# Optimization experiments

Hardware: AMD Instinct MI355X
Metric: run time of the kernel (lower is better)

## Reference

```python
import jax, jax.numpy as jnp
import numpy as np
from jax import lax

N_WIRES = 4
N_OPS = 30
BN_EPS = 1e-5


def _rl_ops():
    # Deterministic stand-in for tq.RandomLayer(n_ops=30): cycle rx/ry/rz/cnot.
    kinds = ['rx', 'ry', 'rz', 'cnot']
    ops, p = [], 0
    for i in range(N_OPS):
        k = kinds[i % 4]
        if k == 'cnot':
            ops.append((k, i % N_WIRES, (i + 1) % N_WIRES))
        else:
            ops.append((k, i % N_WIRES, p))
            p += 1
    return ops, p

RL_OPS, N_RL_PARAMS = _rl_ops()  # 23 rotation params, 7 cnots


def _rx(t):
    c = jnp.cos(t / 2).astype(jnp.complex64)
    s = (-1j * jnp.sin(t / 2).astype(jnp.complex64))
    return jnp.stack([jnp.stack([c, s], -1), jnp.stack([s, c], -1)], -2)


def _ry(t):
    c = jnp.cos(t / 2).astype(jnp.complex64)
    s = jnp.sin(t / 2).astype(jnp.complex64)
    return jnp.stack([jnp.stack([c, -s], -1), jnp.stack([s, c], -1)], -2)


def _rz(t):
    e = jnp.exp((-1j * t / 2).astype(jnp.complex64))
    z = jnp.zeros_like(e)
    return jnp.stack([jnp.stack([e, z], -1), jnp.stack([z, jnp.conj(e)], -1)], -2)


def _apply_1q(state, U, w):
    # state: [B,2,2,2,2]; U: [2,2] (shared) or [B,2,2] (per-sample)
    s = jnp.moveaxis(state, w + 1, -1)
    if U.ndim == 2:
        s = jnp.einsum('ij,b...j->b...i', U, s)
    else:
        s = jnp.einsum('bij,b...j->b...i', U, s)
    return jnp.moveaxis(s, -1, w + 1)


def _apply_cnot(state, c, t):
    s = jnp.moveaxis(state, (c + 1, t + 1), (-2, -1))
    s = s.at[..., 1, :].set(s[..., 1, ::-1])  # flip target where control==1
    return jnp.moveaxis(s, (-2, -1), (c + 1, t + 1))


# PauliZ expectation table: z[k, w] = +/-1 for basis state k on wire w
_ZTAB = np.array([[1.0 - 2.0 * ((k >> (N_WIRES - 1 - w)) & 1) for w in range(N_WIRES)]
                  for k in range(2 ** N_WIRES)], dtype=np.float32)  # [16,4]


def _conv(x, w, b):
    y = lax.conv_general_dilated(x, w, (1, 1), 'SAME',
                                 dimension_numbers=('NCHW', 'OIHW', 'NCHW'))
    return y + b[None, :, None, None]


def _maxpool2(x):
    return lax.reduce_window(x, -jnp.inf, lax.max, (1, 1, 2, 2), (1, 1, 2, 2), 'VALID')


def setup_inputs() -> dict:
    key = jax.random.key(0)
    ks = jax.random.split(key, 8)
    B = 8192
    return {
        'x': jax.random.normal(ks[0], (B, 1, 28, 28), jnp.float32),
        'conv1_w': jax.random.normal(ks[1], (8, 1, 3, 3), jnp.float32) * 0.1,
        'conv1_b': jnp.zeros((8,), jnp.float32),
        'conv2_w': jax.random.normal(ks[2], (16, 8, 3, 3), jnp.float32) * 0.1,
        'conv2_b': jnp.zeros((16,), jnp.float32),
        'fc1_w': jax.random.normal(ks[3], (64, 784), jnp.float32) * 0.05,
        'fc1_b': jnp.zeros((64,), jnp.float32),
        'fc2_w': jax.random.normal(ks[4], (4, 64), jnp.float32) * 0.1,
        'fc2_b': jnp.zeros((4,), jnp.float32),
        'bn_g': jnp.ones((4,), jnp.float32),
        'bn_b': jnp.zeros((4,), jnp.float32),
        'rl_params': jax.random.uniform(ks[5], (N_RL_PARAMS,), jnp.float32,
                                        -np.pi, np.pi),
    }


def reference(x, conv1_w, conv1_b, conv2_w, conv2_b, fc1_w, fc1_b,
              fc2_w, fc2_b, bn_g, bn_b, rl_params):
    B = x.shape[0]
    # CNN backbone: conv -> relu -> pool -> conv -> relu -> pool
    h = _maxpool2(jax.nn.relu(_conv(x, conv1_w, conv1_b)))          # [B,8,14,14]
    h = _maxpool2(jax.nn.relu(_conv(h, conv2_w, conv2_b)))          # [B,16,7,7]
    flat = h.reshape(B, -1)                                         # [B,784]
    h = jax.nn.relu(flat @ fc1_w.T + fc1_b)                         # [B,64]
    feat = h @ fc2_w.T + fc2_b                                      # [B,4]
    # BatchNorm1d (training mode: batch stats, biased variance)
    mean = feat.mean(0)
    var = feat.var(0)
    feat = (feat - mean) / jnp.sqrt(var + BN_EPS) * bn_g + bn_b
    # Quantum state-vector simulation on 4 wires, |0000> start
    state = jnp.zeros((B, 16), jnp.complex64).at[:, 0].set(1.0)
    state = state.reshape(B, 2, 2, 2, 2)
    # Encoder: RX(feat[:, w]) on wire w
    for w in range(N_WIRES):
        state = _apply_1q(state, _rx(feat[:, w]), w)
    # Random layer: 30 sequential gates with fixed trainable params
    gate_fns = {'rx': _rx, 'ry': _ry, 'rz': _rz}
    for kind, w, q in RL_OPS:
        if kind == 'cnot':
            state = _apply_cnot(state, w, q)
        else:
            state = _apply_1q(state, gate_fns[kind](rl_params[q]), w)
    # MeasureAll(PauliZ)
    probs = jnp.abs(state.reshape(B, 16)) ** 2                      # [B,16]
    return probs @ jnp.asarray(_ZTAB)                               # [B,4]
```

## Files before the change

### kernel.cpp

```cpp
#include <hip/hip_runtime.h>
#include <hip/hip_bf16.h>


#define B_EPS 1e-5f

__global__ void prep_kernel(const float* __restrict__ rl,
                            const float* __restrict__ f1w,
                            float* __restrict__ Uout,
                            float* __restrict__ wT2,
                            float* __restrict__ stats)
{
    if (blockIdx.x == 0) {
        __shared__ float2 U[16][16];
        int t = threadIdx.x;
        int r = t >> 4, cc = t & 15;
        U[r][cc] = (r == cc) ? make_float2(1.f, 0.f) : make_float2(0.f, 0.f);
        stats[t] = 0.f;
        stats[t + 256] = 0.f;
        __syncthreads();
        for (int op = 0; op < 30; op++) {
            int kind = op & 3;
            float2 cur = U[r][cc];
            float2 nv;
            if (kind == 3) {
                float2 part = U[r ^ 8][cc];
                nv = (r & 1) ? part : cur;
            } else {
                int m = 8 >> kind;
                float theta = rl[op - (op >> 2)];
                float ch = cosf(0.5f * theta), sh = sinf(0.5f * theta);
                float2 part = U[r ^ m][cc];
                int br = (r & m) ? 1 : 0;
                float2 gc, gp;
                if (kind == 0)      { gc = make_float2(ch, 0.f);           gp = make_float2(0.f, -sh); }
                else if (kind == 1) { gc = make_float2(ch, 0.f);           gp = make_float2(br ? sh : -sh, 0.f); }
                else                { gc = make_float2(ch, br ? sh : -sh); gp = make_float2(0.f, 0.f); }
                nv.x = gc.x*cur.x - gc.y*cur.y + gp.x*part.x - gp.y*part.y;
                nv.y = gc.x*cur.y + gc.y*cur.x + gp.x*part.y + gp.y*part.x;
            }
            __syncthreads();
            U[r][cc] = nv;
            __syncthreads();
        }
        ((float2*)Uout)[t] = U[r][cc];
    } else {
        int id = (blockIdx.x - 1) * 256 + threadIdx.x;
        if (id < 784 * 64) {
            int k = id >> 6, o = id & 63;
            wT2[(((k >> 2) * 64 + o) << 2) + (k & 3)] = f1w[o * 784 + k];
        }
    }
}

__global__ __launch_bounds__(256) void conv_kernel(
    const float* __restrict__ x,  const float* __restrict__ c1w,
    const float* __restrict__ c1b, const float* __restrict__ c2w,
    const float* __restrict__ c2b, const float* __restrict__ wT2,
    const float* __restrict__ f1b, const float* __restrict__ f2w,
    const float* __restrict__ f2bias, float* __restrict__ feat,
    float* __restrict__ stats)
{
    __shared__ union alignas(16) {
        float xin[2][30 * 32];
        float flat[2][800];
    } u;
    __shared__ union alignas(16) {
        float p1[2][8 * 292];
        struct { float part[4][64]; float hs[2][64]; } fc;
    } pu;
    __shared__ float w1s[8][9], b1s[8], w2s[16][73], b2s[16];

    int t = threadIdx.x;
    int w = t >> 6, lane = t & 63;

    {
        float4 z = make_float4(0.f, 0.f, 0.f, 0.f);
        float4* xz = (float4*)u.xin;
        for (int i = t; i < 2 * 30 * 32 / 4; i += 256) xz[i] = z;
        float4* pz = (float4*)pu.p1;
        for (int i = t; i < 2 * 8 * 292 / 4; i += 256) pz[i] = z;
    }
    if (t < 72) ((float*)w1s)[t] = c1w[t];
    if (t < 8)  b1s[t] = c1b[t];
    for (int i = t; i < 16 * 72; i += 256) w2s[i / 72][i % 72] = c2w[i];
    if (t < 16) b2s[t] = c2b[t];
    __syncthreads();

    {
        const float4* xg = (const float4*)(x + (size_t)blockIdx.x * 2 * 784);
        for (int i = t; i < 392; i += 256) {
            float4 v = xg[i];
            int s = i / 196, q = (i - s * 196) * 4;
            float vv[4] = {v.x, v.y, v.z, v.w};
            #pragma unroll
            for (int j = 0; j < 4; j++) {
                int p = q + j, rr = p / 28, cc = p - rr * 28;
                u.xin[s][(rr + 1) * 32 + cc + 1] = vv[j];
            }
        }
    }
    __syncthreads();

    {
        int s = w >> 1, h = w & 1;
        int c = lane >> 3, g = lane & 7;
        if (g < 7) {
            float wk[9];
            #pragma unroll
            for (int q = 0; q < 9; q++) wk[q] = w1s[c][q];
            float bias = b1s[c];
            const float* xb = &u.xin[s][4 * g];
            float* pout = &pu.p1[s][c * 292];
            for (int ii = 0; ii < 7; ii++) {
                int i = h * 7 + ii;
                const float* r = xb + 2 * i * 32;
                float rv[4][6];
                #pragma unroll
                for (int dr = 0; dr < 4; dr++) {
                    float2 a = *(const float2*)(r + dr * 32);
                    float2 b = *(const float2*)(r + dr * 32 + 2);
                    float2 c2v = *(const float2*)(r + dr * 32 + 4);
                    rv[dr][0] = a.x;  rv[dr][1] = a.y;
                    rv[dr][2] = b.x;  rv[dr][3] = b.y;
                    rv[dr][4] = c2v.x; rv[dr][5] = c2v.y;
                }
                float o[2][4];
                #pragma unroll
                for (int dr = 0; dr < 2; dr++)
                    #pragma unroll
                    for (int j = 0; j < 4; j++) {
                        float acc = bias;
                        #pragma unroll
                        for (int ky = 0; ky < 3; ky++)
                            #pragma unroll
                            for (int kx = 0; kx < 3; kx++)
                                acc = fmaf(wk[ky * 3 + kx], rv[dr + ky][j + kx], acc);
                        o[dr][j] = acc;
                    }
                #pragma unroll
                for (int jj = 0; jj < 2; jj++) {
                    float m = fmaxf(fmaxf(o[0][2 * jj], o[0][2 * jj + 1]),
                                    fmaxf(o[1][2 * jj], o[1][2 * jj + 1]));
                    pout[(i + 1) * 18 + 1 + 2 * g + jj] = fmaxf(m, 0.f);
                }
            }
        }
    }
    __syncthreads();

    {
        int s = w >> 1, h = w & 1;
        int c2 = lane >> 2, g2 = lane & 3;
        int i0 = h * 4;
        float bias = b2s[c2];
        float acc[4][2][4];
        #pragma unroll
        for (int ii = 0; ii < 4; ii++)
            #pragma unroll
            for (int dr = 0; dr < 2; dr++)
                #pragma unroll
                for (int j = 0; j < 4; j++) acc[ii][dr][j] = bias;

        const float* pbase = &pu.p1[s][4 * g2] + i0 * 2 * 18;
        for (int ci = 0; ci < 8; ci++) {
            float wk[9];
            #pragma unroll
            for (int q = 0; q < 9; q++) wk[q] = w2s[c2][ci * 9 + q];
            const float* pc_ = pbase + ci * 292;
            #pragma unroll
            for (int ii = 0; ii < 4; ii++) {
                if (ii < 3 || h == 0) {
                    float rv[4][6];
                    #pragma unroll
                    for (int dr = 0; dr < 4; dr++) {
                        const float* rp = pc_ + (ii * 2 + dr) * 18;
                        float2 a = *(const float2*)rp;
                        float2 b = *(const float2*)(rp + 2);
                        float2 cc = *(const float2*)(rp + 4);
                        rv[dr][0] = a.x;  rv[dr][1] = a.y;
                        rv[dr][2] = b.x;  rv[dr][3] = b.y;
                        rv[dr][4] = cc.x; rv[dr][5] = cc.y;
                    }
                    #pragma unroll
                    for (int dr = 0; dr < 2; dr++)
                        #pragma unroll
                        for (int j = 0; j < 4; j++) {
                            float a2 = acc[ii][dr][j];
                            #pragma unroll
                            for (int ky = 0; ky < 3; ky++)
                                #pragma unroll
                                for (int kx = 0; kx < 3; kx++)
                                    a2 = fmaf(wk[ky * 3 + kx], rv[dr + ky][j + kx], a2);
                            acc[ii][dr][j] = a2;
                        }
                }
            }
        }
        #pragma unroll
        for (int ii = 0; ii < 4; ii++) {
            if (ii < 3 || h == 0) {
                int i = i0 + ii;
                #pragma unroll
                for (int jj = 0; jj < 2; jj++) {
                    int pc = 2 * g2 + jj;
                    if (pc < 7) {
                        float m = fmaxf(fmaxf(acc[ii][0][2 * jj], acc[ii][0][2 * jj + 1]),
                                        fmaxf(acc[ii][1][2 * jj], acc[ii][1][2 * jj + 1]));
                        u.flat[s][c2 * 49 + i * 7 + pc] = fmaxf(m, 0.f);
                    }
                }
            }
        }
    }
    __syncthreads();

    {
        int s = w >> 1, h2 = w & 1;
        const float* fl = u.flat[s];
        const float4* wp4 = (const float4*)wT2 + lane;
        int g0 = h2 * 98;
        float a0 = 0.f, a1 = 0.f;
        #pragma unroll 2
        for (int g = g0; g < g0 + 98; g += 2) {
            float4 wv0 = wp4[(size_t)g * 64];
            float4 f0 = *(const float4*)&fl[4 * g];
            float4 wv1 = wp4[(size_t)(g + 1) * 64];
            float4 f1 = *(const float4*)&fl[4 * (g + 1)];
            a0 = fmaf(f0.x, wv0.x, fmaf(f0.y, wv0.y, fmaf(f0.z, wv0.z, fmaf(f0.w, wv0.w, a0))));
            a1 = fmaf(f1.x, wv1.x, fmaf(f1.y, wv1.y, fmaf(f1.z, wv1.z, fmaf(f1.w, wv1.w, a1))));
        }
        pu.fc.part[w][lane] = a0 + a1;
    }
    __syncthreads();

    if (t < 128) {
        int s = t >> 6, o = t & 63;
        float h = pu.fc.part[2 * s][o] + pu.fc.part[2 * s + 1][o] + f1b[o];
        pu.fc.hs[s][o] = fmaxf(h, 0.f);
    }
    __syncthreads();

    if (t < 8) {
        int s = t >> 2, j = t & 3;
        float a = f2bias[j];
        #pragma unroll
        for (int o = 0; o < 64; o++) a = fmaf(pu.fc.hs[s][o], f2w[j * 64 + o], a);
        feat[((size_t)blockIdx.x * 2 + s) * 4 + j] = a;
        int g = blockIdx.x & 63;
        atomicAdd(&stats[g * 8 + j], a);
        atomicAdd(&stats[g * 8 + 4 + j], a * a);
    }
}

__global__ __launch_bounds__(128) void quantum_kernel(
    const float* __restrict__ feat, const float* __restrict__ Ug,
    const float* __restrict__ stats, const float* __restrict__ bn_g,
    const float* __restrict__ bn_b, float* __restrict__ out, int B)
{
    __shared__ float2 Us[256];
    __shared__ float sm[8];
    int t = threadIdx.x;
    for (int i = t; i < 256; i += 128) Us[i] = ((const float2*)Ug)[i];
    if (t < 8) sm[t] = 0.f;
    __syncthreads();
    {
        float v = stats[t] + stats[t + 128] + stats[t + 256] + stats[t + 384];
        atomicAdd(&sm[t & 7], v);
    }
    __syncthreads();
    int s = blockIdx.x * 128 + t;
    float4 fv = ((const float4*)feat)[s];
    float f[4] = {fv.x, fv.y, fv.z, fv.w};
    float cn[4], sn[4];
    float invB = 1.0f / (float)B;
    #pragma unroll
    for (int w = 0; w < 4; w++) {
        float mean = sm[w] * invB;
        float var  = sm[4 + w] * invB - mean * mean;
        float fh = (f[w] - mean) / sqrtf(var + B_EPS) * bn_g[w] + bn_b[w];
        cn[w] = cosf(0.5f * fh);
        sn[w] = sinf(0.5f * fh);
    }
    float re0[16], im0[16];
    #pragma unroll
    for (int k = 0; k < 16; k++) {
        float mag = ((k & 8) ? sn[0] : cn[0]) * ((k & 4) ? sn[1] : cn[1]) *
                    ((k & 2) ? sn[2] : cn[2]) * ((k & 1) ? sn[3] : cn[3]);
        int m = __popc(k) & 3;
        re0[k] = (m == 0) ? mag : (m == 2) ? -mag : 0.f;
        im0[k] = (m == 1) ? -mag : (m == 3) ? mag : 0.f;
    }
    float o0 = 0.f, o1 = 0.f, o2 = 0.f, o3 = 0.f;
    #pragma unroll
    for (int r = 0; r < 16; r++) {
        float ar = 0.f, ai = 0.f;
        #pragma unroll
        for (int k = 0; k < 16; k++) {
            float2 uu = Us[r * 16 + k];
            ar += uu.x * re0[k] - uu.y * im0[k];
            ai += uu.x * im0[k] + uu.y * re0[k];
        }
        float p = ar * ar + ai * ai;
        o0 += (r & 8) ? -p : p;
        o1 += (r & 4) ? -p : p;
        o2 += (r & 2) ? -p : p;
        o3 += (r & 1) ? -p : p;
    }
    float4 ov = {o0, o1, o2, o3};
    ((float4*)out)[s] = ov;
}

extern "C" void kernel_launch(void* const* d_in, const int* in_sizes, int n_in,
                              void* d_out, int out_size, void* d_ws, size_t ws_size,
                              hipStream_t stream)
{
    const float* x   = (const float*)d_in[0];
    const float* c1w = (const float*)d_in[1];
    const float* c1b = (const float*)d_in[2];
    const float* c2w = (const float*)d_in[3];
    const float* c2b = (const float*)d_in[4];
    const float* f1w = (const float*)d_in[5];
    const float* f1b = (const float*)d_in[6];
    const float* f2w = (const float*)d_in[7];
    const float* f2b = (const float*)d_in[8];
    const float* bng = (const float*)d_in[9];
    const float* bnb = (const float*)d_in[10];
    const float* rl  = (const float*)d_in[11];
    float* out = (float*)d_out;

    int B = in_sizes[0] / 784;

    float* wsf   = (float*)d_ws;
    float* feat  = wsf;
    float* wT2   = feat + (size_t)B * 4;
    float* U     = wT2 + 784 * 64;
    float* stats = U + 512;

    prep_kernel<<<197, 256, 0, stream>>>(rl, f1w, U, wT2, stats);
    conv_kernel<<<B / 2, 256, 0, stream>>>(x, c1w, c1b, c2w, c2b, wT2,
                                           f1b, f2w, f2b, feat, stats);
    quantum_kernel<<<B / 128, 128, 0, stream>>>(feat, U, stats, bng, bnb, out, B);
}
```

Before: 226.6 us.

## Run conv2 as an implicit GEMM on MFMA f16 with packed channel layout

New measurement: 235.2 us. +3.8%, slower.

```diff
diff --git a/kernel.cpp b/kernel.cpp
--- a/kernel.cpp
+++ b/kernel.cpp
@@ -3,6 +3,15 @@
 
 
 #define B_EPS 1e-5f
+
+typedef __attribute__((ext_vector_type(8))) _Float16 half8;
+typedef __attribute__((ext_vector_type(4))) float f32x4;
+
+__device__ inline unsigned pack2h(float lo, float hi) {
+    _Float16 l = (_Float16)lo, h = (_Float16)hi;
+    return (unsigned)__builtin_bit_cast(unsigned short, l) |
+           ((unsigned)__builtin_bit_cast(unsigned short, h) << 16);
+}
 
 __global__ void prep_kernel(const float* __restrict__ rl,
                             const float* __restrict__ f1w,
@@ -62,13 +71,18 @@
 {
     __shared__ union alignas(16) {
         float xin[2][30 * 32];
-        float flat[2][800];
+        struct {
+            _Float16 p1c[2][288 * 8];
+            float flat[2][784];
+        } b;
     } u;
     __shared__ union alignas(16) {
         float p1[2][8 * 292];
+        float c2out[196 * 16];
         struct { float part[4][64]; float hs[2][64]; } fc;
-    } pu;
-    __shared__ float w1s[8][9], b1s[8], w2s[16][73], b2s[16];
+    } v;
+    __shared__ unsigned w2c[12 * 16 * 4];
+    __shared__ float w1s[8][9], b1s[8], b2s[16];
 
     int t = threadIdx.x;
     int w = t >> 6, lane = t & 63;
@@ -77,21 +91,25 @@
         float4 z = make_float4(0.f, 0.f, 0.f, 0.f);
         float4* xz = (float4*)u.xin;
         for (int i = t; i < 2 * 30 * 32 / 4; i += 256) xz[i] = z;
-        float4* pz = (float4*)pu.p1;
+        float4* pz = (float4*)v.p1;
         for (int i = t; i < 2 * 8 * 292 / 4; i += 256) pz[i] = z;
     }
     if (t < 72) ((float*)w1s)[t] = c1w[t];
     if (t < 8)  b1s[t] = c1b[t];
-    for (int i = t; i < 16 * 72; i += 256) w2s[i / 72][i % 72] = c2w[i];
-    if (t < 16) b2s[t] = c2b[t];
-    __syncthreads();
-
+    if (t >= 8 && t < 24) b2s[t - 8] = c2b[t - 8];
+    for (int j = t; j < 576; j += 256) {
+        int tap = j >> 6, r = j & 63, ch = r >> 2, ci2 = r & 3;
+        float lo = c2w[ch * 72 + (2 * ci2) * 9 + tap];
+        float hi = c2w[ch * 72 + (2 * ci2 + 1) * 9 + tap];
+        w2c[(tap * 16 + ch) * 4 + ci2] = pack2h(lo, hi);
+    }
+    if (t < 192) w2c[576 + t] = 0u;
     {
         const float4* xg = (const float4*)(x + (size_t)blockIdx.x * 2 * 784);
         for (int i = t; i < 392; i += 256) {
-            float4 v = xg[i];
+            float4 vv4 = xg[i];
             int s = i / 196, q = (i - s * 196) * 4;
-            float vv[4] = {v.x, v.y, v.z, v.w};
+            float vv[4] = {vv4.x, vv4.y, vv4.z, vv4.w};
             #pragma unroll
             for (int j = 0; j < 4; j++) {
                 int p = q + j, rr = p / 28, cc = p - rr * 28;
@@ -110,7 +128,7 @@
             for (int q = 0; q < 9; q++) wk[q] = w1s[c][q];
             float bias = b1s[c];
             const float* xb = &u.xin[s][4 * g];
-            float* pout = &pu.p1[s][c * 292];
+            float* pout = &v.p1[s][c * 292];
             for (int ii = 0; ii < 7; ii++) {
                 int i = h * 7 + ii;
                 const float* r = xb + 2 * i * 32;
@@ -149,74 +167,109 @@
     __syncthreads();
 
     {
-        int s = w >> 1, h = w & 1;
-        int c2 = lane >> 2, g2 = lane & 3;
-        int i0 = h * 4;
-        float bias = b2s[c2];
-        float acc[4][2][4];
+        unsigned* pc = (unsigned*)u.b.p1c;
+        for (int i = t; i < 2304; i += 256) {
+            int s = i / 1152, r = i - 1152 * s;
+            int pix = r >> 2, c2 = r & 3;
+            float lo = v.p1[s][(2 * c2) * 292 + pix];
+            float hi = v.p1[s][(2 * c2 + 1) * 292 + pix];
+            pc[i] = pack2h(lo, hi);
+        }
+    }
+    __syncthreads();
+
+    int q = lane >> 4, n = lane & 15;
+    int okm, alpha[4], gamma[4];
+    {
+        const _Float16 one = (_Float16)1.0f;
+        const _Float16 enc = (_Float16)(float)(n + 1);
+        const half8 z8 = {0,0,0,0,0,0,0,0};
+        const f32x4 z4 = {0.f, 0.f, 0.f, 0.f};
+        half8 aa, bb;
+        f32x4 Pa, Pb, Pc, Pd, Pe, Pf;
+        aa = z8; bb = z8; if (q == 0) { aa[0] = enc; bb[0] = one; }
+        Pa = __builtin_amdgcn_mfma_f32_16x16x32_f16(aa, bb, z4, 0, 0, 0);
+        aa = z8; bb = z8; if (q == 0) { aa[5] = enc; bb[5] = one; }
+        Pb = __builtin_amdgcn_mfma_f32_16x16x32_f16(aa, bb, z4, 0, 0, 0);
+        aa = z8; bb = z8; if (q == 2) { aa[6] = enc; bb[6] = one; }
+        Pe = __builtin_amdgcn_mfma_f32_16x16x32_f16(aa, bb, z4, 0, 0, 0);
+        aa = z8; bb = z8; if (q == 3) { aa[3] = enc; bb[3] = one; }
+        Pf = __builtin_amdgcn_mfma_f32_16x16x32_f16(aa, bb, z4, 0, 0, 0);
+        aa = z8; bb = z8; if (q == 0) { aa[0] = one; bb[0] = enc; }
+        Pc = __builtin_amdgcn_mfma_f32_16x16x32_f16(aa, bb, z4, 0, 0, 0);
+        aa = z8; bb = z8; if (q == 1) { aa[1] = one; bb[1] = enc; }
+        Pd = __builtin_amdgcn_mfma_f32_16x16x32_f16(aa, bb, z4, 0, 0, 0);
+        int ok = 1;
         #pragma unroll
-        for (int ii = 0; ii < 4; ii++)
+        for (int e = 0; e < 4; e++) {
+            int a1 = (int)(Pa[e] + 0.5f);
+            int g1 = (int)(Pc[e] + 0.5f);
+            ok &= (a1 >= 1) & (a1 <= 16) & (g1 >= 1) & (g1 <= 16);
+            ok &= (fabsf(Pb[e] - Pa[e]) < 0.5f) & (fabsf(Pe[e] - Pa[e]) < 0.5f)
+                & (fabsf(Pf[e] - Pa[e]) < 0.5f) & (fabsf(Pd[e] - Pc[e]) < 0.5f);
+            alpha[e] = a1 - 1;
+            gamma[e] = g1 - 1;
+        }
+        okm = __all(ok);
+    }
+
+    for (int s = 0; s < 2; s++) {
+        if (okm) {
+            half8 bfr[3];
+            int atoff[3];
             #pragma unroll
-            for (int dr = 0; dr < 2; dr++)
-                #pragma unroll
-                for (int j = 0; j < 4; j++) acc[ii][dr][j] = bias;
-
-        const float* pbase = &pu.p1[s][4 * g2] + i0 * 2 * 18;
-        for (int ci = 0; ci < 8; ci++) {
-            float wk[9];
-            #pragma unroll
-            for (int q = 0; q < 9; q++) wk[q] = w2s[c2][ci * 9 + q];
-            const float* pc_ = pbase + ci * 292;
-            #pragma unroll
-            for (int ii = 0; ii < 4; ii++) {
-                if (ii < 3 || h == 0) {
-                    float rv[4][6];
+            for (int s2 = 0; s2 < 3; s2++) {
+                int tap = 4 * s2 + q;
+                bfr[s2] = *(const half8*)&w2c[(tap * 16 + n) * 4];
+                atoff[s2] = (tap < 9) ? ((tap / 3) * 18 + (tap % 3)) * 8 : 0;
+            }
+            for (int tau = w; tau < 13; tau += 4) {
+                int r0 = tau * 16 + n;
+                int rp = r0 < 196 ? r0 : 0;
+                int oy = rp / 14, ox = rp - 14 * oy;
+                const _Float16* ab = &u.b.p1c[s][(oy * 18 + ox) * 8];
+                f32x4 acc = {0.f, 0.f, 0.f, 0.f};
+                acc = __builtin_amdgcn_mfma_f32_16x16x32_f16(*(const half8*)(ab + atoff[0]), bfr[0], acc, 0, 0, 0);
+                acc = __builtin_amdgcn_mfma_f32_16x16x32_f16(*(const half8*)(ab + atoff[1]), bfr[1], acc, 0, 0, 0);
+                acc = __builtin_amdgcn_mfma_f32_16x16x32_f16(*(const half8*)(ab + atoff[2]), bfr[2], acc, 0, 0, 0);
+                #pragma unroll
+                for (int e = 0; e < 4; e++) {
+                    int pix = tau * 16 + alpha[e];
+                    if (pix < 196) v.c2out[pix * 16 + gamma[e]] = acc[e];
+                }
+            }
+        } else {
+            for (int idx = t; idx < 3136; idx += 256) {
+                int pix = idx >> 4, ch = idx & 15;
+                int oy = pix / 14, ox = pix - 14 * oy;
+                float acc = 0.f;
+                #pragma unroll
+                for (int tap = 0; tap < 9; tap++) {
+                    const half8 av = *(const half8*)&u.b.p1c[s][((oy + tap / 3) * 18 + ox + tap % 3) * 8];
+                    const half8 wv = *(const half8*)&w2c[(tap * 16 + ch) * 4];
                     #pragma unroll
-                    for (int dr = 0; dr < 4; dr++) {
-                        const float* rp = pc_ + (ii * 2 + dr) * 18;
-                        float2 a = *(const float2*)rp;
-                        float2 b = *(const float2*)(rp + 2);
-                        float2 cc = *(const float2*)(rp + 4);
-                        rv[dr][0] = a.x;  rv[dr][1] = a.y;
-                        rv[dr][2] = b.x;  rv[dr][3] = b.y;
-                        rv[dr][4] = cc.x; rv[dr][5] = cc.y;
-                    }
-                    #pragma unroll
-                    for (int dr = 0; dr < 2; dr++)
-                        #pragma unroll
-                        for (int j = 0; j < 4; j++) {
-                            float a2 = acc[ii][dr][j];
-                            #pragma unroll
-                            for (int ky = 0; ky < 3; ky++)
-                                #pragma unroll
-                                for (int kx = 0; kx < 3; kx++)
-                                    a2 = fmaf(wk[ky * 3 + kx], rv[dr + ky][j + kx], a2);
-                            acc[ii][dr][j] = a2;
-                        }
+                    for (int j = 0; j < 8; j++)
+                        acc = fmaf((float)av[j], (float)wv[j], acc);
                 }
-            }
-        }
-        #pragma unroll
-        for (int ii = 0; ii < 4; ii++) {
-            if (ii < 3 || h == 0) {
-                int i = i0 + ii;
-                #pragma unroll
-                for (int jj = 0; jj < 2; jj++) {
-                    int pc = 2 * g2 + jj;
-                    if (pc < 7) {
-                        float m = fmaxf(fmaxf(acc[ii][0][2 * jj], acc[ii][0][2 * jj + 1]),
-                                        fmaxf(acc[ii][1][2 * jj], acc[ii][1][2 * jj + 1]));
-                        u.flat[s][c2 * 49 + i * 7 + pc] = fmaxf(m, 0.f);
-                    }
-                }
-            }
-        }
-    }
-    __syncthreads();
+                v.c2out[pix * 16 + ch] = acc;
+            }
+        }
+        __syncthreads();
+        for (int idx = t; idx < 784; idx += 256) {
+            int ch = idx / 49, g = idx - 49 * ch;
+            int gy = g / 7, gx = g - 7 * gy;
+            const float* cb = &v.c2out[((2 * gy) * 14 + 2 * gx) * 16 + ch];
+            float v0 = cb[0], v1 = cb[16];
+            float v2 = cb[224], v3 = cb[240];
+            float m = fmaxf(fmaxf(v0, v1), fmaxf(v2, v3));
+            u.b.flat[s][idx] = fmaxf(m + b2s[ch], 0.f);
+        }
+        __syncthreads();
+    }
 
     {
         int s = w >> 1, h2 = w & 1;
-        const float* fl = u.flat[s];
+        const float* fl = u.b.flat[s];
         const float4* wp4 = (const float4*)wT2 + lane;
         int g0 = h2 * 98;
         float a0 = 0.f, a1 = 0.f;
@@ -229,14 +282,14 @@
             a0 = fmaf(f0.x, wv0.x, fmaf(f0.y, wv0.y, fmaf(f0.z, wv0.z, fmaf(f0.w, wv0.w, a0))));
             a1 = fmaf(f1.x, wv1.x, fmaf(f1.y, wv1.y, fmaf(f1.z, wv1.z, fmaf(f1.w, wv1.w, a1))));
         }
-        pu.fc.part[w][lane] = a0 + a1;
+        v.fc.part[w][lane] = a0 + a1;
     }
     __syncthreads();
 
     if (t < 128) {
         int s = t >> 6, o = t & 63;
-        float h = pu.fc.part[2 * s][o] + pu.fc.part[2 * s + 1][o] + f1b[o];
-        pu.fc.hs[s][o] = fmaxf(h, 0.f);
+        float h = v.fc.part[2 * s][o] + v.fc.part[2 * s + 1][o] + f1b[o];
+        v.fc.hs[s][o] = fmaxf(h, 0.f);
     }
     __syncthreads();
 
@@ -244,7 +297,7 @@
         int s = t >> 2, j = t & 3;
         float a = f2bias[j];
         #pragma unroll
-        for (int o = 0; o < 64; o++) a = fmaf(pu.fc.hs[s][o], f2w[j * 64 + o], a);
+        for (int o = 0; o < 64; o++) a = fmaf(v.fc.hs[s][o], f2w[j * 64 + o], a);
         feat[((size_t)blockIdx.x * 2 + s) * 4 + j] = a;
         int g = blockIdx.x & 63;
         atomicAdd(&stats[g * 8 + j], a);
```
